# Optimization experiments

Hardware: AMD Instinct MI355X
Metric: run time of the kernel (lower is better)

## Reference

```python
import math
import jax, jax.numpy as jnp
import numpy as np

DIM = 1024
FFN_DIM = 4096
NUM_HEADS = 16
HEAD_DIM = DIM // NUM_HEADS
SCALE = 1.0 / math.sqrt(HEAD_DIM)
EPS = 1e-5


def _layer_norm(x, gamma, beta):
    mu = jnp.mean(x, axis=-1, keepdims=True)
    var = jnp.mean(jnp.square(x - mu), axis=-1, keepdims=True)
    return (x - mu) * jax.lax.rsqrt(var + EPS) * gamma + beta


def _gelu_erf(x):
    # matches torch GELU module: x * 0.5 * (1 + erf(x / sqrt(2)))
    return x * 0.5 * (1.0 + jax.lax.erf(x / math.sqrt(2.0)))


def setup_inputs() -> dict:
    key = jax.random.key(0)
    ks = jax.random.split(key, 12)
    B, L = 2, 2048
    s = 0.02
    inp = {
        "x": jax.random.normal(ks[0], (B, L, DIM), dtype=jnp.float32),
        "g1": jnp.ones((DIM,), jnp.float32),
        "b1": jnp.zeros((DIM,), jnp.float32),
        "Wq": jax.random.normal(ks[1], (DIM, DIM), jnp.float32) * s,
        "bq": jnp.zeros((DIM,), jnp.float32),
        "Wk": jax.random.normal(ks[2], (DIM, DIM), jnp.float32) * s,
        "bk": jnp.zeros((DIM,), jnp.float32),
        "Wv": jax.random.normal(ks[3], (DIM, DIM), jnp.float32) * s,
        "bv": jnp.zeros((DIM,), jnp.float32),
        "Wo": jax.random.normal(ks[4], (DIM, DIM), jnp.float32) * s,
        "bo": jnp.zeros((DIM,), jnp.float32),
        "g2": jnp.ones((DIM,), jnp.float32),
        "b2": jnp.zeros((DIM,), jnp.float32),
        "W1": jax.random.normal(ks[5], (FFN_DIM, DIM), jnp.float32) * s,
        "bf1": jnp.zeros((FFN_DIM,), jnp.float32),
        "W2": jax.random.normal(ks[6], (DIM, FFN_DIM), jnp.float32) * s,
        "bf2": jnp.zeros((DIM,), jnp.float32),
    }
    return inp


def reference(x, g1, b1, Wq, bq, Wk, bk, Wv, bv, Wo, bo, g2, b2, W1, bf1, W2, bf2):
    B, L, C = x.shape
    n, c = NUM_HEADS, HEAD_DIM

    # ---- pre-norm self-attention ----
    h = _layer_norm(x, g1, b1)
    q = (h @ Wq.T + bq).reshape(B, L, n, c)
    k = (h @ Wk.T + bk).reshape(B, L, n, c)
    v = (h @ Wv.T + bv).reshape(B, L, n, c)
    attn = SCALE * jnp.einsum('binc,bjnc->bnij', q, k)   # [B, n, L, L]
    attn = jax.nn.softmax(attn, axis=-1)
    o = jnp.einsum('bnij,bjnc->binc', attn, v).reshape(B, L, C)
    x = x + (o @ Wo.T + bo)

    # ---- pre-norm FFN (GELU, erf form) ----
    h = _layer_norm(x, g2, b2)
    h = _gelu_erf(h @ W1.T + bf1)
    x = x + (h @ W2.T + bf2)
    return x
```

## Files before the change

### kernel.cpp

```cpp
#include <hip/hip_runtime.h>
#include <hip/hip_bf16.h>
#include <math.h>

typedef unsigned short u16;
typedef __attribute__((ext_vector_type(8))) __bf16 bf16x8;
typedef __attribute__((ext_vector_type(4))) float f32x4;

#define DIM   1024
#define LSEQ  2048
#define BTOK  4096
#define HD    64
#define FFN   4096
#define QSCL  0.18033688011112042f

#if __has_builtin(__builtin_amdgcn_exp2f)
#define EXP2(x) __builtin_amdgcn_exp2f(x)
#else
#define EXP2(x) exp2f(x)
#endif

__device__ __forceinline__ u16 f2bf(float f) {
  unsigned u = __builtin_bit_cast(unsigned, f);
  u += 0x7FFFu + ((u >> 16) & 1u);
  return (u16)(u >> 16);
}
__device__ __forceinline__ unsigned pk2(float a, float b) {
  return (unsigned)f2bf(a) | ((unsigned)f2bf(b) << 16);
}
__device__ __forceinline__ unsigned cvtpk(float lo, float hi) {
  unsigned r;
  asm("v_cvt_pk_bf16_f32 %0, %1, %2" : "=v"(r) : "v"(lo), "v"(hi));
  return r;
}
__device__ __forceinline__ f32x4 mfma16(bf16x8 a, bf16x8 b, f32x4 c) {
  return __builtin_amdgcn_mfma_f32_16x16x32_bf16(a, b, c, 0, 0, 0);
}
__device__ __forceinline__ void gload16(const void* g, void* l) {
  __builtin_amdgcn_global_load_lds((const __attribute__((address_space(1))) char*)g,
                                   (__attribute__((address_space(3))) char*)l, 16, 0, 0);
}
__device__ __forceinline__ float gelu_t(float v) {
  float v3 = v * v * v;
  float tt = fmaf(-0.10296766f, v3, -2.30258509f * v);
  return v * __builtin_amdgcn_rcpf(1.0f + EXP2(tt));
}

__global__ __launch_bounds__(256) void ln_kernel(const float* __restrict__ x,
                                                 const float* __restrict__ g,
                                                 const float* __restrict__ bta,
                                                 u16* __restrict__ out) {
  int row = blockIdx.x, t = threadIdx.x;
  const float* xr = x + (size_t)row * DIM;
  float4 xv = *(const float4*)(xr + t * 4);
  float s  = xv.x + xv.y + xv.z + xv.w;
  float ss = xv.x * xv.x + xv.y * xv.y + xv.z * xv.z + xv.w * xv.w;
#pragma unroll
  for (int m = 32; m >= 1; m >>= 1) {
    s  += __shfl_xor(s, m);
    ss += __shfl_xor(ss, m);
  }
  __shared__ float red[8];
  if ((t & 63) == 0) { red[(t >> 6) * 2] = s; red[(t >> 6) * 2 + 1] = ss; }
  __syncthreads();
  s  = red[0] + red[2] + red[4] + red[6];
  ss = red[1] + red[3] + red[5] + red[7];
  float mu  = s * (1.0f / DIM);
  float var = ss * (1.0f / DIM) - mu * mu;
  float rs  = rsqrtf(var + 1e-5f);
  float4 gv = *(const float4*)(g + t * 4);
  float4 bv = *(const float4*)(bta + t * 4);
  uint2 o;
  o.x = pk2((xv.x - mu) * rs * gv.x + bv.x, (xv.y - mu) * rs * gv.y + bv.y);
  o.y = pk2((xv.z - mu) * rs * gv.z + bv.z, (xv.w - mu) * rs * gv.w + bv.w);
  *(uint2*)(out + (size_t)row * DIM + t * 4) = o;
}

__global__ __launch_bounds__(256) void wcvt4(const float* __restrict__ Wq, const float* __restrict__ Wk,
                                             const float* __restrict__ Wv, const float* __restrict__ Wo,
                                             u16* __restrict__ dst) {
  int b = blockIdx.x;
  int r = b >> 9;
  const float* s = (r == 0) ? Wq : (r == 1) ? Wk : (r == 2) ? Wv : Wo;
  size_t i = (((size_t)(b & 511)) * 256 + threadIdx.x) * 8;
  float4 f0 = *(const float4*)(s + i), f1 = *(const float4*)(s + i + 4);
  uint4 o = { pk2(f0.x, f0.y), pk2(f0.z, f0.w), pk2(f1.x, f1.y), pk2(f1.z, f1.w) };
  *(uint4*)(dst + ((size_t)r << 20) + i) = o;
}
__global__ __launch_bounds__(256) void wcvt2(const float* __restrict__ W1, const float* __restrict__ W2,
                                             u16* __restrict__ d1, u16* __restrict__ d2) {
  int b = blockIdx.x;
  const float* s = (b < 2048) ? W1 : W2;
  u16* d = (b < 2048) ? d1 : d2;
  size_t i = (((size_t)(b & 2047)) * 256 + threadIdx.x) * 8;
  float4 f0 = *(const float4*)(s + i), f1 = *(const float4*)(s + i + 4);
  uint4 o = { pk2(f0.x, f0.y), pk2(f0.z, f0.w), pk2(f1.x, f1.y), pk2(f1.z, f1.w) };
  *(uint4*)(d + i) = o;
}

__global__ __launch_bounds__(256) void transpose_v(const u16* __restrict__ v,
                                                   u16* __restrict__ vt) {
  __shared__ u16 tls[64][80];
  int jb = blockIdx.x, bh = blockIdx.y, b = bh >> 4, h = bh & 15;
  int t = threadIdx.x;
  int r = t >> 2, seg = t & 3;
  const u16* src = v + (size_t)(b * LSEQ + jb * 64 + r) * DIM + h * HD + seg * 16;
  *(uint4*)&tls[r][seg * 16]     = *(const uint4*)src;
  *(uint4*)&tls[r][seg * 16 + 8] = *(const uint4*)(src + 8);
  __syncthreads();
  int c = t >> 2, jseg = t & 3;
  u16 tmp[16] __attribute__((aligned(16)));
#pragma unroll
  for (int i = 0; i < 16; i++) tmp[i] = tls[jseg * 16 + i][c];
  u16* dst = vt + ((size_t)bh * HD + c) * LSEQ + jb * 64 + jseg * 16;
  *(uint4*)dst       = *(const uint4*)tmp;
  *(uint4*)(dst + 8) = *(const uint4*)(tmp + 8);
}

struct GArg { const u16* Wb; const float* bias; u16* outB; float oscale; };

template <int EPI, int BM>
__global__ __launch_bounds__(256) void gemm3(const u16* __restrict__ A,
                                             GArg g0, GArg g1, GArg g2,
                                             const float* __restrict__ resid,
                                             float* __restrict__ outF,
                                             int N, int K, int nbPerW) {
  constexpr int WM = BM / 32;
  constexpr int ABUF = BM * 64;
  __shared__ u16 lsa[2][BM * 32];
  __shared__ u16 lsb[2][128 * 32];
  const int t = threadIdx.x;
  const int w = t >> 6, l = t & 63, l15 = l & 15, lg = l >> 4;
  const int wr = w >> 1, wc = w & 1;
  const int nwg = gridDim.x * gridDim.y;
  int flat = blockIdx.y * gridDim.x + blockIdx.x;
  flat = (flat & 7) * (nwg >> 3) + (flat >> 3);
  const int bx = flat % gridDim.x, by = flat / gridDim.x;
  const int sel = bx / nbPerW, nb = bx % nbPerW;
  GArg G = (sel == 0) ? g0 : ((sel == 1) ? g1 : g2);
  const int n0 = nb * 128, m0 = by * BM;

  f32x4 acc[WM][4];
#pragma unroll
  for (int m = 0; m < WM; m++)
#pragma unroll
    for (int n = 0; n < 4; n++) acc[m][n] = (f32x4){0.f, 0.f, 0.f, 0.f};

  const int grow = t >> 2;
  const int gcol = 8 * ((t & 3) ^ ((t >> 3) & 3));
  const u16* Asrc = A + (size_t)(m0 + grow) * K + gcol;
  const u16* Bsrc = G.Wb + (size_t)(n0 + grow) * K + gcol;
  const int rs = (l15 >> 1) & 3;

  const char* aadr = (const char*)lsa + (wr * (BM / 2) + l15) * 64 + (lg ^ rs) * 16;
  const char* badr = (const char*)lsb + (wc * 64 + l15) * 64 + (lg ^ rs) * 16;

  auto stage = [&](int k0, int buf) {
#pragma unroll
    for (int i = 0; i < BM / 64; i++)
      gload16(Asrc + (size_t)i * 64 * K + k0, (char*)lsa + buf * ABUF + i * 4096 + w * 1024);
#pragma unroll
    for (int i = 0; i < 2; i++)
      gload16(Bsrc + (size_t)i * 64 * K + k0, (char*)lsb + buf * 8192 + i * 4096 + w * 1024);
  };

  stage(0, 0);
  const int NT = K >> 5;
  for (int it = 0; it < NT; it++) {
    const int buf = it & 1;
    __syncthreads();
    if (it + 1 < NT) stage((it + 1) << 5, buf ^ 1);

    const char* ap = aadr + buf * ABUF;
    const char* bp = badr + buf * 8192;
    bf16x8 af[WM], bfr[4];
#pragma unroll
    for (int m = 0; m < WM; m++)
      af[m] = *(const bf16x8*)(ap + m * 1024);
#pragma unroll
    for (int n = 0; n < 4; n++)
      bfr[n] = *(const bf16x8*)(bp + n * 1024);
#pragma unroll
    for (int m = 0; m < WM; m++)
#pragma unroll
      for (int n = 0; n < 4; n++)
        acc[m][n] = mfma16(af[m], bfr[n], acc[m][n]);
  }

#pragma unroll
  for (int m = 0; m < WM; m++) {
    const int row = m0 + wr * (BM / 2) + m * 16 + lg * 4;
#pragma unroll
    for (int n = 0; n < 4; n++) {
      const int col = n0 + wc * 64 + n * 16 + l15;
      const float bias = G.bias[col];
#pragma unroll
      for (int r = 0; r < 4; r++) {
        const float v = acc[m][n][r] + bias;
        const size_t idx = (size_t)(row + r) * N + col;
        if (EPI == 0)      G.outB[idx] = f2bf(v * G.oscale);
        else if (EPI == 1) outF[idx] = v + resid[idx];
        else               G.outB[idx] = f2bf(gelu_t(v));
      }
    }
  }
}

__global__ __launch_bounds__(128, 2) void attn6(const u16* __restrict__ q,
                                                const u16* __restrict__ k,
                                                const u16* __restrict__ vt,
                                                u16* __restrict__ o) {
  __shared__ __align__(16) char smem[40960];
  const int t = threadIdx.x, w = t >> 6, l = t & 63, l15 = l & 15, lg = l >> 4;
  int flat = blockIdx.y * gridDim.x + blockIdx.x;
  flat = (flat & 7) * 128 + (flat >> 3);
  const int qbk = flat & 31, bh = flat >> 5;
  const int b = bh >> 4, h = bh & 15;
  const int qrow0 = b * LSEQ + qbk * 64 + w * 32;
  const int r7 = l15 & 7;
  const int c0 = lg ^ r7;

  bf16x8 av[2][2];
#pragma unroll
  for (int m = 0; m < 2; m++)
#pragma unroll
    for (int i = 0; i < 2; i++)
      av[m][i] = *(const bf16x8*)(q + (size_t)(qrow0 + m * 16 + l15) * DIM + h * HD + i * 32 + lg * 8);

  const char* adrA  = smem + l15 * 128 + c0 * 16;
  const char* adrB  = smem + l15 * 128 + (c0 ^ 4) * 16;
  const char* padrA = smem + 32768 + w * 4096 + l15 * 128 + c0 * 16;
  const char* padrB = smem + 32768 + w * 4096 + l15 * 128 + (c0 ^ 4) * 16;
  char* pwa[4];
#pragma unroll
  for (int cb = 0; cb < 4; cb++)
    pwa[cb] = smem + 32768 + w * 4096 + l15 * 128 +
              (((2 * cb + (lg >> 1)) ^ r7) * 16) + (lg & 1) * 8;

  const int srow = l >> 3;
  const int schk = 8 * ((l & 7) ^ (srow & 7));
  const u16* ksrc = k + (size_t)(b * LSEQ + w * 32 + srow) * DIM + h * HD + schk;
  const u16* vsrc = vt + ((size_t)bh * HD + w * 32 + srow) * LSEQ + schk;

  f32x4 oacc[2][4];
#pragma unroll
  for (int m = 0; m < 2; m++)
#pragma unroll
    for (int cb = 0; cb < 4; cb++) oacc[m][cb] = (f32x4){0.f, 0.f, 0.f, 0.f};
  f32x4 minit[2] = {(f32x4){0.f, 0.f, 0.f, 0.f}, (f32x4){0.f, 0.f, 0.f, 0.f}};
  float lsum[2] = {0.f, 0.f};

  auto issueTile = [&](int jt, int buf) {
    const u16* kp = ksrc + (size_t)jt * DIM;
    const u16* vp = vsrc + jt;
#pragma unroll
    for (int j = 0; j < 4; j++) {
      gload16(kp + (size_t)j * 8 * DIM,  smem + buf * 8192 + w * 4096 + j * 1024);
      gload16(vp + (size_t)j * 8 * LSEQ, smem + 16384 + buf * 8192 + w * 4096 + j * 1024);
    }
  };

  issueTile(0, 0);
  for (int it = 0; it < LSEQ / 64; it++) {
    const int buf = it & 1;
    __syncthreads();
    if (it + 1 < LSEQ / 64) issueTile((it + 1) * 64, buf ^ 1);
    const int ko = buf * 8192;

    f32x4 s[2][4];
    const char* kA = adrA + ko;
    const char* kB = adrB + ko;
    __builtin_amdgcn_s_setprio(1);
#pragma unroll
    for (int cb = 0; cb < 4; cb++) {
      bf16x8 kf0 = *(const bf16x8*)(kA + cb * 2048);
      bf16x8 kf1 = *(const bf16x8*)(kB + cb * 2048);
      s[0][cb] = mfma16(kf0, av[0][0], minit[0]);
      s[1][cb] = mfma16(kf0, av[1][0], minit[1]);
      s[0][cb] = mfma16(kf1, av[0][1], s[0][cb]);
      s[1][cb] = mfma16(kf1, av[1][1], s[1][cb]);
    }
    __builtin_amdgcn_s_setprio(0);

    float tm[2];
#pragma unroll
    for (int m = 0; m < 2; m++)
      tm[m] = fmaxf(fmaxf(fmaxf(s[m][0][0], s[m][0][1]), fmaxf(s[m][0][2], s[m][0][3])),
                    fmaxf(fmaxf(fmaxf(s[m][1][0], s[m][1][1]), fmaxf(s[m][1][2], s[m][1][3])),
                          fmaxf(fmaxf(fmaxf(s[m][2][0], s[m][2][1]), fmaxf(s[m][2][2], s[m][2][3])),
                                fmaxf(fmaxf(s[m][3][0], s[m][3][1]), fmaxf(s[m][3][2], s[m][3][3])))));
    if (__any(fmaxf(tm[0], tm[1]) > 8.0f)) {
#pragma unroll
      for (int m = 0; m < 2; m++) {
        float tr = fmaxf(tm[m], __shfl_xor(tm[m], 16));
        tr = fmaxf(tr, __shfl_xor(tr, 32));
        const float d = fmaxf(tr, 0.f);
        const float scl = EXP2(-d);
        const f32x4 dv = (f32x4){d, d, d, d};
        lsum[m] *= scl;
        minit[m] -= dv;
#pragma unroll
        for (int cb = 0; cb < 4; cb++) s[m][cb] -= dv;
#pragma unroll
        for (int r = 0; r < 4; r++) {
          const float so = __shfl(scl, lg * 4 + r);
#pragma unroll
          for (int cb = 0; cb < 4; cb++) oacc[m][cb][r] *= so;
        }
      }
    }
#pragma unroll
    for (int m = 0; m < 2; m++) {
      float ps = 0.f;
      uint2 pk[4];
#pragma unroll
      for (int cb = 0; cb < 4; cb++) {
        float a0 = EXP2(s[m][cb][0]);
        float a1 = EXP2(s[m][cb][1]);
        float a2 = EXP2(s[m][cb][2]);
        float a3 = EXP2(s[m][cb][3]);
        ps += (a0 + a1) + (a2 + a3);
        pk[cb].x = cvtpk(a0, a1);
        pk[cb].y = cvtpk(a2, a3);
      }
      lsum[m] += ps;
#pragma unroll
      for (int cb = 0; cb < 4; cb++) *(uint2*)(pwa[cb] + m * 2048) = pk[cb];
    }

    const char* vA = adrA + ko + 16384;
    const char* vB = adrB + ko + 16384;
    bf16x8 pa0[2], pa1[2];
#pragma unroll
    for (int m = 0; m < 2; m++) {
      pa0[m] = *(const bf16x8*)(padrA + m * 2048);
      pa1[m] = *(const bf16x8*)(padrB + m * 2048);
    }
    __builtin_amdgcn_s_setprio(1);
#pragma unroll
    for (int cb = 0; cb < 4; cb++) {
      bf16x8 vf0 = *(const bf16x8*)(vA + cb * 2048);
      oacc[0][cb] = mfma16(pa0[0], vf0, oacc[0][cb]);
      oacc[1][cb] = mfma16(pa0[1], vf0, oacc[1][cb]);
    }
#pragma unroll
    for (int cb = 0; cb < 4; cb++) {
      bf16x8 vf1 = *(const bf16x8*)(vB + cb * 2048);
      oacc[0][cb] = mfma16(pa1[0], vf1, oacc[0][cb]);
      oacc[1][cb] = mfma16(pa1[1], vf1, oacc[1][cb]);
    }
    __builtin_amdgcn_s_setprio(0);
  }

#pragma unroll
  for (int m = 0; m < 2; m++) {
    float rl = lsum[m] + __shfl_xor(lsum[m], 16);
    rl += __shfl_xor(rl, 32);
#pragma unroll
    for (int r = 0; r < 4; r++) {
      const float lo = __shfl(rl, lg * 4 + r);
      const float rcp = 1.0f / lo;
#pragma unroll
      for (int cb = 0; cb < 4; cb++) {
        o[(size_t)(qrow0 + m * 16 + lg * 4 + r) * DIM + h * HD + cb * 16 + l15] =
            f2bf(oacc[m][cb][r] * rcp);
      }
    }
  }
}

extern "C" void kernel_launch(void* const* d_in, const int* in_sizes, int n_in,
                              void* d_out, int out_size, void* d_ws, size_t ws_size,
                              hipStream_t stream) {
  const float* x   = (const float*)d_in[0];
  const float* g1  = (const float*)d_in[1];
  const float* b1  = (const float*)d_in[2];
  const float* Wq  = (const float*)d_in[3];
  const float* bq  = (const float*)d_in[4];
  const float* Wk  = (const float*)d_in[5];
  const float* bk  = (const float*)d_in[6];
  const float* Wv  = (const float*)d_in[7];
  const float* bv  = (const float*)d_in[8];
  const float* Wo  = (const float*)d_in[9];
  const float* bo  = (const float*)d_in[10];
  const float* g2  = (const float*)d_in[11];
  const float* b2  = (const float*)d_in[12];
  const float* W1  = (const float*)d_in[13];
  const float* bf1 = (const float*)d_in[14];
  const float* W2  = (const float*)d_in[15];
  const float* bf2 = (const float*)d_in[16];
  float* out = (float*)d_out;

  const size_t E = (size_t)BTOK * DIM;
  u16* h     = (u16*)d_ws;
  u16* qb    = h + E;
  u16* kbuf  = qb + E;
  u16* vbuf  = kbuf + E;
  u16* vtb   = vbuf + E;
  u16* wqkvo = vtb + E;
  u16* ob    = vbuf;
  u16* W1b   = qb;
  u16* W2b   = kbuf;
  u16* mid   = vbuf;
  u16* h2    = h;
  float* x2  = out;

  u16* Wqb = wqkvo;
  u16* Wkb = wqkvo + ((size_t)1 << 20);
  u16* Wvb = wqkvo + ((size_t)2 << 20);
  u16* Wob = wqkvo + ((size_t)3 << 20);

  wcvt4<<<dim3(2048), dim3(256), 0, stream>>>(Wq, Wk, Wv, Wo, wqkvo);
  ln_kernel<<<dim3(BTOK), dim3(256), 0, stream>>>(x, g1, b1, h);
  gemm3<0, 128><<<dim3(24, BTOK / 128), 256, 0, stream>>>(
      h, GArg{Wqb, bq, qb, QSCL}, GArg{Wkb, bk, kbuf, 1.0f}, GArg{Wvb, bv, vbuf, 1.0f},
      nullptr, nullptr, DIM, DIM, 8);
  transpose_v<<<dim3(32, 32), 256, 0, stream>>>(vbuf, vtb);
  attn6<<<dim3(LSEQ / 64, 32), 128, 0, stream>>>(qb, kbuf, vtb, ob);
  {
    GArg s{Wob, bo, nullptr, 1.0f};
    gemm3<1, 64><<<dim3(8, BTOK / 64), 256, 0, stream>>>(ob, s, s, s, x, x2, DIM, DIM, 8);
  }
  wcvt2<<<dim3(4096), dim3(256), 0, stream>>>(W1, W2, W1b, W2b);
  ln_kernel<<<dim3(BTOK), dim3(256), 0, stream>>>(x2, g2, b2, h2);
  {
    GArg s{W1b, bf1, mid, 1.0f};
    gemm3<2, 128><<<dim3(32, BTOK / 128), 256, 0, stream>>>(h2, s, s, s, nullptr, nullptr, FFN, DIM, 32);
  }
  {
    GArg s{W2b, bf2, nullptr, 1.0f};
    gemm3<1, 64><<<dim3(8, BTOK / 64), 256, 0, stream>>>(mid, s, s, s, x2, out, DIM, FFN, 8);
  }
}
```

Baseline: 254.5 us.

## Add double-buffered 64x128 GEMM kernel for residual projections

```diff
diff --git a/kernel.cpp b/kernel.cpp
--- a/kernel.cpp
+++ b/kernel.cpp
@@ -200,6 +200,97 @@
         if (EPI == 0)      G.outB[idx] = f2bf(v * G.oscale);
         else if (EPI == 1) outF[idx] = v + resid[idx];
         else               G.outB[idx] = f2bf(gelu_t(v));
+      }
+    }
+  }
+}
+
+__global__ __launch_bounds__(256) void gemm5(const u16* __restrict__ A,
+                                             const u16* __restrict__ W,
+                                             const float* __restrict__ bias,
+                                             const float* __restrict__ resid,
+                                             float* __restrict__ outF,
+                                             int N, int K) {
+  __shared__ u16 lsa[2][64 * 64];
+  __shared__ u16 lsb[2][128 * 64];
+  const int t = threadIdx.x;
+  const int w = t >> 6, l = t & 63, l15 = l & 15, lg = l >> 4;
+  const int wr = w >> 1, wc = w & 1;
+  const int nwg = gridDim.x * gridDim.y;
+  int flat = blockIdx.y * gridDim.x + blockIdx.x;
+  flat = (flat & 7) * (nwg >> 3) + (flat >> 3);
+  const int bx = flat % gridDim.x, by = flat / gridDim.x;
+  const int n0 = bx * 128, m0 = by * 64;
+
+  f32x4 acc[2][4];
+#pragma unroll
+  for (int m = 0; m < 2; m++)
+#pragma unroll
+    for (int n = 0; n < 4; n++) acc[m][n] = (f32x4){0.f, 0.f, 0.f, 0.f};
+
+  const int srow = w * 8 + (l >> 3);
+  const int scol = 8 * ((l & 7) ^ ((l >> 3) & 7));
+  const u16* Asrc = A + (size_t)(m0 + srow) * K + scol;
+  const u16* Bsrc = W + (size_t)(n0 + srow) * K + scol;
+
+  const int r3 = l15 & 3, rb = (l15 >> 2) & 1;
+  const int cA = lg ^ r3;
+  const char* abase = (const char*)lsa + (wr * 32 + l15) * 128;
+  const char* bbase = (const char*)lsb + (wc * 64 + l15) * 128;
+  const char* aadr0 = abase + ((rb)     * 4 + cA) * 16;
+  const char* aadr1 = abase + ((rb ^ 1) * 4 + cA) * 16;
+  const char* badr0 = bbase + ((rb)     * 4 + cA) * 16;
+  const char* badr1 = bbase + ((rb ^ 1) * 4 + cA) * 16;
+
+  auto stage = [&](int k0, int buf) {
+#pragma unroll
+    for (int i = 0; i < 2; i++)
+      gload16(Asrc + (size_t)i * 32 * K + k0, (char*)lsa + buf * 8192 + i * 4096 + w * 1024);
+#pragma unroll
+    for (int i = 0; i < 4; i++)
+      gload16(Bsrc + (size_t)i * 32 * K + k0, (char*)lsb + buf * 16384 + i * 4096 + w * 1024);
+  };
+
+  stage(0, 0);
+  const int NT = K >> 6;
+  for (int it = 0; it < NT; it++) {
+    const int buf = it & 1;
+    __syncthreads();
+    if (it + 1 < NT) stage((it + 1) << 6, buf ^ 1);
+
+    const int ao = buf * 8192;
+    const int bo = buf * 16384;
+    bf16x8 af[2][2], bfr[4][2];
+#pragma unroll
+    for (int m = 0; m < 2; m++) {
+      af[m][0] = *(const bf16x8*)(aadr0 + ao + m * 2048);
+      af[m][1] = *(const bf16x8*)(aadr1 + ao + m * 2048);
+    }
+#pragma unroll
+    for (int n = 0; n < 4; n++) {
+      bfr[n][0] = *(const bf16x8*)(badr0 + bo + n * 2048);
+      bfr[n][1] = *(const bf16x8*)(badr1 + bo + n * 2048);
+    }
+#pragma unroll
+    for (int m = 0; m < 2; m++)
+#pragma unroll
+      for (int n = 0; n < 4; n++) {
+        acc[m][n] = mfma16(af[m][0], bfr[n][0], acc[m][n]);
+        acc[m][n] = mfma16(af[m][1], bfr[n][1], acc[m][n]);
+      }
+  }
+
+#pragma unroll
+  for (int m = 0; m < 2; m++) {
+    const int row = m0 + wr * 32 + m * 16 + lg * 4;
+#pragma unroll
+    for (int n = 0; n < 4; n++) {
+      const int col = n0 + wc * 64 + n * 16 + l15;
+      const float bc = bias[col];
+#pragma unroll
+      for (int r = 0; r < 4; r++) {
+        const size_t idx = (size_t)(row + r) * N + col;
+        outF[idx] = acc[m][n][r] + bc + resid[idx];
       }
     }
   }
@@ -416,18 +507,12 @@
       nullptr, nullptr, DIM, DIM, 8);
   transpose_v<<<dim3(32, 32), 256, 0, stream>>>(vbuf, vtb);
   attn6<<<dim3(LSEQ / 64, 32), 128, 0, stream>>>(qb, kbuf, vtb, ob);
-  {
-    GArg s{Wob, bo, nullptr, 1.0f};
-    gemm3<1, 64><<<dim3(8, BTOK / 64), 256, 0, stream>>>(ob, s, s, s, x, x2, DIM, DIM, 8);
-  }
+  gemm5<<<dim3(8, BTOK / 64), 256, 0, stream>>>(ob, Wob, bo, x, x2, DIM, DIM);
   wcvt2<<<dim3(4096), dim3(256), 0, stream>>>(W1, W2, W1b, W2b);
   ln_kernel<<<dim3(BTOK), dim3(256), 0, stream>>>(x2, g2, b2, h2);
   {
     GArg s{W1b, bf1, mid, 1.0f};
     gemm3<2, 128><<<dim3(32, BTOK / 128), 256, 0, stream>>>(h2, s, s, s, nullptr, nullptr, FFN, DIM, 32);
   }
-  {
-    GArg s{W2b, bf2, nullptr, 1.0f};
-    gemm3<1, 64><<<dim3(8, BTOK / 64), 256, 0, stream>>>(mid, s, s, s, x2, out, DIM, FFN, 8);
-  }
-}
+  gemm5<<<dim3(8, BTOK / 64), 256, 0, stream>>>(mid, W2b, bf2, x2, out, DIM, FFN);
+}
```

New measurement: 243.4 us. 4.4% less time.

## Double GEMM K-tile to 64 and widen attention blocks to 128 query rows

Applied to the files above, without the earlier changes.

```diff
diff --git a/kernel.cpp b/kernel.cpp
--- a/kernel.cpp
+++ b/kernel.cpp
@@ -119,15 +119,15 @@
 struct GArg { const u16* Wb; const float* bias; u16* outB; float oscale; };
 
 template <int EPI, int BM>
-__global__ __launch_bounds__(256) void gemm3(const u16* __restrict__ A,
+__global__ __launch_bounds__(256) void gemm6(const u16* __restrict__ A,
                                              GArg g0, GArg g1, GArg g2,
                                              const float* __restrict__ resid,
                                              float* __restrict__ outF,
                                              int N, int K, int nbPerW) {
-  constexpr int WM = BM / 32;
-  constexpr int ABUF = BM * 64;
-  __shared__ u16 lsa[2][BM * 32];
-  __shared__ u16 lsb[2][128 * 32];
+  constexpr int WM   = BM / 32;
+  constexpr int ABUF = BM * 128;
+  __shared__ u16 lsa[2][BM * 64];
+  __shared__ u16 lsb[2][128 * 64];
   const int t = threadIdx.x;
   const int w = t >> 6, l = t & 63, l15 = l & 15, lg = l >> 4;
   const int wr = w >> 1, wc = w & 1;
@@ -145,45 +145,56 @@
 #pragma unroll
     for (int n = 0; n < 4; n++) acc[m][n] = (f32x4){0.f, 0.f, 0.f, 0.f};
 
-  const int grow = t >> 2;
-  const int gcol = 8 * ((t & 3) ^ ((t >> 3) & 3));
-  const u16* Asrc = A + (size_t)(m0 + grow) * K + gcol;
-  const u16* Bsrc = G.Wb + (size_t)(n0 + grow) * K + gcol;
-  const int rs = (l15 >> 1) & 3;
-
-  const char* aadr = (const char*)lsa + (wr * (BM / 2) + l15) * 64 + (lg ^ rs) * 16;
-  const char* badr = (const char*)lsb + (wc * 64 + l15) * 64 + (lg ^ rs) * 16;
+  const int srow = w * 8 + (l >> 3);
+  const int scol = 8 * ((l & 7) ^ ((l >> 3) & 7));
+  const u16* Asrc = A + (size_t)(m0 + srow) * K + scol;
+  const u16* Bsrc = G.Wb + (size_t)(n0 + srow) * K + scol;
+
+  const int r3 = l15 & 3, rb = (l15 >> 2) & 1;
+  const int cA = lg ^ r3;
+  const char* abase = (const char*)lsa + (wr * (BM / 2) + l15) * 128;
+  const char* bbase = (const char*)lsb + (wc * 64 + l15) * 128;
+  const char* aadr0 = abase + ((rb)     * 4 + cA) * 16;
+  const char* aadr1 = abase + ((rb ^ 1) * 4 + cA) * 16;
+  const char* badr0 = bbase + ((rb)     * 4 + cA) * 16;
+  const char* badr1 = bbase + ((rb ^ 1) * 4 + cA) * 16;
 
   auto stage = [&](int k0, int buf) {
 #pragma unroll
-    for (int i = 0; i < BM / 64; i++)
-      gload16(Asrc + (size_t)i * 64 * K + k0, (char*)lsa + buf * ABUF + i * 4096 + w * 1024);
-#pragma unroll
-    for (int i = 0; i < 2; i++)
-      gload16(Bsrc + (size_t)i * 64 * K + k0, (char*)lsb + buf * 8192 + i * 4096 + w * 1024);
+    for (int i = 0; i < BM / 32; i++)
+      gload16(Asrc + (size_t)i * 32 * K + k0, (char*)lsa + buf * ABUF + i * 4096 + w * 1024);
+#pragma unroll
+    for (int i = 0; i < 4; i++)
+      gload16(Bsrc + (size_t)i * 32 * K + k0, (char*)lsb + buf * 16384 + i * 4096 + w * 1024);
   };
 
   stage(0, 0);
-  const int NT = K >> 5;
+  const int NT = K >> 6;
   for (int it = 0; it < NT; it++) {
     const int buf = it & 1;
     __syncthreads();
-    if (it + 1 < NT) stage((it + 1) << 5, buf ^ 1);
-
-    const char* ap = aadr + buf * ABUF;
-    const char* bp = badr + buf * 8192;
-    bf16x8 af[WM], bfr[4];
+    if (it + 1 < NT) stage((it + 1) << 6, buf ^ 1);
+
+    const int ao = buf * ABUF;
+    const int bo = buf * 16384;
+    bf16x8 af[WM][2], bfr[4][2];
+#pragma unroll
+    for (int m = 0; m < WM; m++) {
+      af[m][0] = *(const bf16x8*)(aadr0 + ao + m * 2048);
+      af[m][1] = *(const bf16x8*)(aadr1 + ao + m * 2048);
+    }
+#pragma unroll
+    for (int n = 0; n < 4; n++) {
+      bfr[n][0] = *(const bf16x8*)(badr0 + bo + n * 2048);
+      bfr[n][1] = *(const bf16x8*)(badr1 + bo + n * 2048);
+    }
 #pragma unroll
     for (int m = 0; m < WM; m++)
-      af[m] = *(const bf16x8*)(ap + m * 1024);
-#pragma unroll
-    for (int n = 0; n < 4; n++)
-      bfr[n] = *(const bf16x8*)(bp + n * 1024);
-#pragma unroll
-    for (int m = 0; m < WM; m++)
-#pragma unroll
-      for (int n = 0; n < 4; n++)
-        acc[m][n] = mfma16(af[m], bfr[n], acc[m][n]);
+#pragma unroll
+      for (int n = 0; n < 4; n++) {
+        acc[m][n] = mfma16(af[m][0], bfr[n][0], acc[m][n]);
+        acc[m][n] = mfma16(af[m][1], bfr[n][1], acc[m][n]);
+      }
   }
 
 #pragma unroll
@@ -192,11 +203,11 @@
 #pragma unroll
     for (int n = 0; n < 4; n++) {
       const int col = n0 + wc * 64 + n * 16 + l15;
-      const float bias = G.bias[col];
+      const float bc = G.bias[col];
 #pragma unroll
       for (int r = 0; r < 4; r++) {
-        const float v = acc[m][n][r] + bias;
         const size_t idx = (size_t)(row + r) * N + col;
+        const float v = acc[m][n][r] + bc;
         if (EPI == 0)      G.outB[idx] = f2bf(v * G.oscale);
         else if (EPI == 1) outF[idx] = v + resid[idx];
         else               G.outB[idx] = f2bf(gelu_t(v));
@@ -205,17 +216,17 @@
   }
 }
 
-__global__ __launch_bounds__(128, 2) void attn6(const u16* __restrict__ q,
+__global__ __launch_bounds__(256, 3) void attn7(const u16* __restrict__ q,
                                                 const u16* __restrict__ k,
                                                 const u16* __restrict__ vt,
                                                 u16* __restrict__ o) {
-  __shared__ __align__(16) char smem[40960];
+  __shared__ __align__(16) char smem[49152];
   const int t = threadIdx.x, w = t >> 6, l = t & 63, l15 = l & 15, lg = l >> 4;
   int flat = blockIdx.y * gridDim.x + blockIdx.x;
-  flat = (flat & 7) * 128 + (flat >> 3);
-  const int qbk = flat & 31, bh = flat >> 5;
+  flat = (flat & 7) * 64 + (flat >> 3);
+  const int qbk = flat & 15, bh = flat >> 4;
   const int b = bh >> 4, h = bh & 15;
-  const int qrow0 = b * LSEQ + qbk * 64 + w * 32;
+  const int qrow0 = b * LSEQ + qbk * 128 + w * 32;
   const int r7 = l15 & 7;
   const int c0 = lg ^ r7;
 
@@ -238,8 +249,8 @@
 
   const int srow = l >> 3;
   const int schk = 8 * ((l & 7) ^ (srow & 7));
-  const u16* ksrc = k + (size_t)(b * LSEQ + w * 32 + srow) * DIM + h * HD + schk;
-  const u16* vsrc = vt + ((size_t)bh * HD + w * 32 + srow) * LSEQ + schk;
+  const u16* ksrc = k + (size_t)(b * LSEQ + w * 16 + srow) * DIM + h * HD + schk;
+  const u16* vsrc = vt + ((size_t)bh * HD + w * 16 + srow) * LSEQ + schk;
 
   f32x4 oacc[2][4];
 #pragma unroll
@@ -253,9 +264,9 @@
     const u16* kp = ksrc + (size_t)jt * DIM;
     const u16* vp = vsrc + jt;
 #pragma unroll
-    for (int j = 0; j < 4; j++) {
-      gload16(kp + (size_t)j * 8 * DIM,  smem + buf * 8192 + w * 4096 + j * 1024);
-      gload16(vp + (size_t)j * 8 * LSEQ, smem + 16384 + buf * 8192 + w * 4096 + j * 1024);
+    for (int j = 0; j < 2; j++) {
+      gload16(kp + (size_t)j * 8 * DIM,  smem + buf * 8192 + w * 2048 + j * 1024);
+      gload16(vp + (size_t)j * 8 * LSEQ, smem + 16384 + buf * 8192 + w * 2048 + j * 1024);
     }
   };
 
@@ -411,23 +422,23 @@
 
   wcvt4<<<dim3(2048), dim3(256), 0, stream>>>(Wq, Wk, Wv, Wo, wqkvo);
   ln_kernel<<<dim3(BTOK), dim3(256), 0, stream>>>(x, g1, b1, h);
-  gemm3<0, 128><<<dim3(24, BTOK / 128), 256, 0, stream>>>(
+  gemm6<0, 128><<<dim3(24, BTOK / 128), 256, 0, stream>>>(
       h, GArg{Wqb, bq, qb, QSCL}, GArg{Wkb, bk, kbuf, 1.0f}, GArg{Wvb, bv, vbuf, 1.0f},
       nullptr, nullptr, DIM, DIM, 8);
   transpose_v<<<dim3(32, 32), 256, 0, stream>>>(vbuf, vtb);
-  attn6<<<dim3(LSEQ / 64, 32), 128, 0, stream>>>(qb, kbuf, vtb, ob);
+  attn7<<<dim3(LSEQ / 128, 32), 256, 0, stream>>>(qb, kbuf, vtb, ob);
   {
     GArg s{Wob, bo, nullptr, 1.0f};
-    gemm3<1, 64><<<dim3(8, BTOK / 64), 256, 0, stream>>>(ob, s, s, s, x, x2, DIM, DIM, 8);
+    gemm6<1, 64><<<dim3(8, BTOK / 64), 256, 0, stream>>>(ob, s, s, s, x, x2, DIM, DIM, 8);
   }
   wcvt2<<<dim3(4096), dim3(256), 0, stream>>>(W1, W2, W1b, W2b);
   ln_kernel<<<dim3(BTOK), dim3(256), 0, stream>>>(x2, g2, b2, h2);
   {
     GArg s{W1b, bf1, mid, 1.0f};
-    gemm3<2, 128><<<dim3(32, BTOK / 128), 256, 0, stream>>>(h2, s, s, s, nullptr, nullptr, FFN, DIM, 32);
+    gemm6<2, 128><<<dim3(32, BTOK / 128), 256, 0, stream>>>(h2, s, s, s, nullptr, nullptr, FFN, DIM, 32);
   }
   {
     GArg s{W2b, bf2, nullptr, 1.0f};
-    gemm3<1, 64><<<dim3(8, BTOK / 64), 256, 0, stream>>>(mid, s, s, s, x2, out, DIM, FFN, 8);
-  }
-}
+    gemm6<1, 64><<<dim3(8, BTOK / 64), 256, 0, stream>>>(mid, s, s, s, x2, out, DIM, FFN, 8);
+  }
+}
```

After: 238.1 us. 1.07x faster.
